# Kernel optimization log

Measured on AMD Instinct MI355X. Metric: run time of the kernel, lower is better.

## Reference

```python
import jax, jax.numpy as jnp
import numpy as np

N = 8192      # nodes
E = 262144    # edges per graph (avg degree 32)
D_IN = 256
HID = 64
HEADS = 2
NEG_SLOPE = 0.2  # PyG GATConv leaky_relu slope


def _self_loops(ei, n):
    loop = jnp.arange(n, dtype=ei.dtype)
    return jnp.concatenate([ei[0], loop]), jnp.concatenate([ei[1], loop])


def gat_conv(x, src, dst, W, att_src, att_dst, b, concat):
    # PyG GATConv: h=[N,H,C]; alpha=softmax_dst(leaky_relu(a_s[src]+a_d[dst]))
    n = x.shape[0]
    H, C = att_src.shape
    h = (x @ W).reshape(n, H, C)
    a_s = (h * att_src).sum(-1)           # [N,H]
    a_d = (h * att_dst).sum(-1)           # [N,H]
    e = jax.nn.leaky_relu(a_s[src] + a_d[dst], NEG_SLOPE)  # [Etot,H]
    e = e - jax.ops.segment_max(e, dst, num_segments=n)[dst]
    e = jnp.exp(e)
    denom = jax.ops.segment_sum(e, dst, num_segments=n)[dst] + 1e-16
    alpha = e / denom                     # edge softmax per target node
    msg = h[src] * alpha[:, :, None]      # [Etot,H,C]
    out = jax.ops.segment_sum(msg, dst, num_segments=n)  # [N,H,C]
    out = out.reshape(n, H * C) if concat else out.mean(axis=1)
    return out + b


def gcn_conv(x, src, dst, W, b):
    # PyG GCNConv: D^{-1/2}(A+I)D^{-1/2} X W + b (self loops already appended)
    n = x.shape[0]
    h = x @ W
    deg = jax.ops.segment_sum(jnp.ones_like(src, jnp.float32), dst, num_segments=n)
    dinv = jax.lax.rsqrt(jnp.maximum(deg, 1.0))
    norm = dinv[src] * dinv[dst]          # [Etot]
    return jax.ops.segment_sum(h[src] * norm[:, None], dst, num_segments=n) + b


def cross_attn(q_in, kv_in, Wq, bq, Wk, bk, Wv, bv, Wo, bo, num_heads):
    n, d = q_in.shape
    hd = d // num_heads
    q = (q_in @ Wq + bq).reshape(n, num_heads, hd)
    k = (kv_in @ Wk + bk).reshape(n, num_heads, hd)
    v = (kv_in @ Wv + bv).reshape(n, num_heads, hd)
    scores = jnp.einsum('qhd,khd->hqk', q, k) / np.sqrt(hd).astype(np.float32)
    attn = jax.nn.softmax(scores, axis=-1)                 # [H,N,N]
    out = jnp.einsum('hqk,khd->qhd', attn, v).reshape(n, d) @ Wo + bo
    weights = attn.mean(axis=0)[None]                      # [1,N,N] avg heads (torch default)
    return out, weights


def setup_inputs():
    key = jax.random.key(0)
    ks = jax.random.split(key, 24)
    w = lambda k, s: jax.random.normal(k, s, jnp.float32) * 0.05
    inp = {
        'x': jax.random.normal(ks[0], (N, D_IN), jnp.float32),
        'edge_index_tkg': jax.random.randint(ks[1], (2, E), 0, N, jnp.int64 if jax.config.jax_enable_x64 else jnp.int32),
        'edge_index_ekg': jax.random.randint(ks[2], (2, E), 0, N, jnp.int64 if jax.config.jax_enable_x64 else jnp.int32),
        # GAT layer 1: heads=2, concat=True
        'gat1_W': w(ks[3], (D_IN, HEADS * HID)),
        'gat1_att_src': w(ks[4], (HEADS, HID)),
        'gat1_att_dst': w(ks[5], (HEADS, HID)),
        'gat1_b': jnp.zeros((HEADS * HID,), jnp.float32),
        # GAT layer 2: heads=1, concat=False
        'gat2_W': w(ks[6], (HEADS * HID, HID)),
        'gat2_att_src': w(ks[7], (1, HID)),
        'gat2_att_dst': w(ks[8], (1, HID)),
        'gat2_b': jnp.zeros((HID,), jnp.float32),
        # GCN layers
        'gcn1_W': w(ks[9], (D_IN, HID)),
        'gcn1_b': jnp.zeros((HID,), jnp.float32),
        'gcn2_W': w(ks[10], (HID, HID)),
        'gcn2_b': jnp.zeros((HID,), jnp.float32),
        # cross attention (hidden=64, 2 heads)
        'Wq': w(ks[11], (HID, HID)), 'bq': jnp.zeros((HID,), jnp.float32),
        'Wk': w(ks[12], (HID, HID)), 'bk': jnp.zeros((HID,), jnp.float32),
        'Wv': w(ks[13], (HID, HID)), 'bv': jnp.zeros((HID,), jnp.float32),
        'Wo': w(ks[14], (HID, HID)), 'bo': jnp.zeros((HID,), jnp.float32),
        # MLP head
        'fc1_W': w(ks[15], (2 * HID, HID)), 'fc1_b': jnp.zeros((HID,), jnp.float32),
        'fc2_W': w(ks[16], (HID, 1)), 'fc2_b': jnp.zeros((1,), jnp.float32),
    }
    return inp


def reference(x, edge_index_tkg, edge_index_ekg,
              gat1_W, gat1_att_src, gat1_att_dst, gat1_b,
              gat2_W, gat2_att_src, gat2_att_dst, gat2_b,
              gcn1_W, gcn1_b, gcn2_W, gcn2_b,
              Wq, bq, Wk, bk, Wv, bv, Wo, bo,
              fc1_W, fc1_b, fc2_W, fc2_b):
    n = x.shape[0]
    src_t, dst_t = _self_loops(edge_index_tkg, n)
    src_e, dst_e = _self_loops(edge_index_ekg, n)

    h_tkg = jax.nn.elu(gat_conv(x, src_t, dst_t, gat1_W, gat1_att_src, gat1_att_dst, gat1_b, True))
    h_tkg = jax.nn.elu(gat_conv(h_tkg, src_t, dst_t, gat2_W, gat2_att_src, gat2_att_dst, gat2_b, False))

    h_ekg = jax.nn.relu(gcn_conv(x, src_e, dst_e, gcn1_W, gcn1_b))
    h_ekg = jax.nn.relu(gcn_conv(h_ekg, src_e, dst_e, gcn2_W, gcn2_b))

    h_attn, attn_weights = cross_attn(h_tkg, h_ekg, Wq, bq, Wk, bk, Wv, bv, Wo, bo, HEADS)

    h_fused = jnp.concatenate([h_tkg, h_attn], axis=1)   # [N, 2*HID]
    pred = (jax.nn.relu(h_fused @ fc1_W + fc1_b) @ fc2_W + fc2_b).squeeze(-1)
    return pred, attn_weights
```

## Files before the change

kernel.cpp:

```cpp
#include <hip/hip_runtime.h>
#include <cstdint>
#include <cstddef>

#define NN 8192
#define EE 262144
#define ET 270336

using short8  = __attribute__((ext_vector_type(8))) short;
using floatx4 = __attribute__((ext_vector_type(4))) float;

__device__ __forceinline__ unsigned short f2bf(float f) {
  unsigned int u = __float_as_uint(f);
  u += 0x7fffu + ((u >> 16) & 1u);
  return (unsigned short)(u >> 16);
}

__global__ void edge_hist2_k(const int* __restrict__ ei_t, const int* __restrict__ ei_e,
                             int* __restrict__ cnt_t, int* __restrict__ cnt_e) {
  int idx = blockIdx.x * 256 + threadIdx.x;
  int g = idx >= ET;
  int e = g ? idx - ET : idx;
  const int* ei = g ? ei_e : ei_t;
  int* cnt = g ? cnt_e : cnt_t;
  int d = (e < EE) ? ei[EE + e] : (e - EE);
  atomicAdd(&cnt[d], 1);
}

__global__ void scan2_k(int* cnt_t, int* off_t, int* cnt_e, int* off_e) {
  int* cnt = blockIdx.x ? cnt_e : cnt_t;
  int* off = blockIdx.x ? off_e : off_t;
  __shared__ int s[1024];
  int t = threadIdx.x;
  int v[8]; int base = t * 8; int sum = 0;
  #pragma unroll
  for (int j = 0; j < 8; ++j) { v[j] = cnt[base + j]; sum += v[j]; }
  s[t] = sum; __syncthreads();
  for (int o = 1; o < 1024; o <<= 1) {
    int x = (t >= o) ? s[t - o] : 0;
    __syncthreads();
    s[t] += x;
    __syncthreads();
  }
  int excl = s[t] - sum;
  #pragma unroll
  for (int j = 0; j < 8; ++j) { off[base + j] = excl; cnt[base + j] = excl; excl += v[j]; }
  if (t == 1023) off[NN] = excl;
}

__global__ void edge_scatter2_k(const int* __restrict__ ei_t, const int* __restrict__ ei_e,
                                int* __restrict__ pos_t, int* __restrict__ pos_e,
                                int* __restrict__ srcs_t, int* __restrict__ srcs_e) {
  int idx = blockIdx.x * 256 + threadIdx.x;
  int g = idx >= ET;
  int e = g ? idx - ET : idx;
  const int* ei = g ? ei_e : ei_t;
  int* pos = g ? pos_e : pos_t;
  int* srcs = g ? srcs_e : srcs_t;
  int sv, d;
  if (e < EE) { sv = ei[e]; d = ei[EE + e]; } else { sv = d = e - EE; }
  int p = atomicAdd(&pos[d], 1);
  srcs[p] = sv;
}

__device__ __forceinline__ void gemm_core(const float* __restrict__ A, int lda, int K,
                                          const float* __restrict__ Bs, int row0, int col,
                                          float acc[8]) {
  #pragma unroll
  for (int r = 0; r < 8; ++r) acc[r] = 0.f;
  for (int k = 0; k < K; k += 4) {
    float b0 = Bs[(k + 0) * 32 + col], b1 = Bs[(k + 1) * 32 + col];
    float b2 = Bs[(k + 2) * 32 + col], b3 = Bs[(k + 3) * 32 + col];
    #pragma unroll
    for (int r = 0; r < 8; ++r) {
      const float4 a4 = *(const float4*)(A + (size_t)(row0 + r) * lda + k);
      acc[r] = fmaf(a4.x, b0, acc[r]);
      acc[r] = fmaf(a4.y, b1, acc[r]);
      acc[r] = fmaf(a4.z, b2, acc[r]);
      acc[r] = fmaf(a4.w, b3, acc[r]);
    }
  }
}

__global__ __launch_bounds__(256) void mm_x_k(const float* __restrict__ x,
    const float* __restrict__ Wgat, const float* __restrict__ Wgcn,
    const float* __restrict__ as_w, const float* __restrict__ ad_w,
    float* __restrict__ h1, float* __restrict__ hg1,
    float* __restrict__ a_s1, float* __restrict__ a_d1) {
  __shared__ float Bs[256 * 32];
  const int tid = threadIdx.x, by = blockIdx.y;
  const bool gat = by < 4;
  const int NC = gat ? 128 : 64;
  const int c0 = gat ? by * 32 : (by - 4) * 32;
  const float* B = gat ? Wgat : Wgcn;
  for (int idx = tid; idx < 256 * 32; idx += 256)
    Bs[idx] = B[(idx >> 5) * NC + c0 + (idx & 31)];
  __syncthreads();
  const int row0 = blockIdx.x * 64 + (tid >> 5) * 8;
  const int col = tid & 31;
  float acc[8];
  gemm_core(x, 256, 256, Bs, row0, col, acc);
  if (gat) {
    #pragma unroll
    for (int r = 0; r < 8; ++r) h1[(size_t)(row0 + r) * 128 + c0 + col] = acc[r];
    const int head = c0 >> 6;
    const float asw = as_w[head * 64 + (c0 & 63) + col];
    const float adw = ad_w[head * 64 + (c0 & 63) + col];
    float ps[8], pd[8];
    #pragma unroll
    for (int r = 0; r < 8; ++r) { ps[r] = acc[r] * asw; pd[r] = acc[r] * adw; }
    #pragma unroll
    for (int m = 16; m >= 1; m >>= 1)
      #pragma unroll
      for (int r = 0; r < 8; ++r) { ps[r] += __shfl_xor(ps[r], m); pd[r] += __shfl_xor(pd[r], m); }
    if (col == 0) {
      #pragma unroll
      for (int r = 0; r < 8; ++r) {
        atomicAdd(&a_s1[(row0 + r) * 2 + head], ps[r]);
        atomicAdd(&a_d1[(row0 + r) * 2 + head], pd[r]);
      }
    }
  } else {
    #pragma unroll
    for (int r = 0; r < 8; ++r) hg1[(size_t)(row0 + r) * 64 + c0 + col] = acc[r];
  }
}

template<int H, int C>
__device__ __forceinline__ void gat_agg_body(const float* __restrict__ h,
    const float* __restrict__ a_s, const float* __restrict__ a_d,
    const int* __restrict__ off, const int* __restrict__ srcs,
    const float* __restrict__ bias, float* __restrict__ out, int ldout, int b) {
  constexpr int HC = H * C;
  const int tid = threadIdx.x;
  const int hd = tid / C;
  const int r0 = off[b], r1 = off[b + 1];
  __shared__ int s_src[HC];
  __shared__ float s_w[HC][H];
  float ad[H];
  #pragma unroll
  for (int hh = 0; hh < H; ++hh) ad[hh] = a_d[b * H + hh];
  float acc = 0.f, den = 0.f;
  for (int base = r0; base < r1; base += HC) {
    __syncthreads();
    int e = base + tid;
    if (e < r1) {
      int sv = srcs[e];
      s_src[tid] = sv;
      #pragma unroll
      for (int hh = 0; hh < H; ++hh) {
        float xv = a_s[sv * H + hh] + ad[hh];
        xv = xv > 0.f ? xv : 0.2f * xv;
        s_w[tid][hh] = __expf(xv);
      }
    }
    __syncthreads();
    int cnt = min(HC, r1 - base);
    for (int j = 0; j < cnt; ++j) {
      float wv = s_w[j][hd];
      den += wv;
      acc = fmaf(wv, h[(size_t)s_src[j] * HC + tid], acc);
    }
  }
  float o = acc / den + bias[tid];
  out[(size_t)b * ldout + tid] = o > 0.f ? o : (__expf(o) - 1.f);
}

template<int H, int C>
__global__ void gat_agg_k(const float* __restrict__ h, const float* __restrict__ a_s,
                          const float* __restrict__ a_d, const int* __restrict__ off,
                          const int* __restrict__ srcs, const float* __restrict__ bias,
                          float* __restrict__ out, int ldout) {
  gat_agg_body<H, C>(h, a_s, a_d, off, srcs, bias, out, ldout, blockIdx.x);
}

__global__ __launch_bounds__(128) void agg1_k(
    const float* __restrict__ h1, const float* __restrict__ a_s1, const float* __restrict__ a_d1,
    const int* __restrict__ off_t, const int* __restrict__ src_t,
    const float* __restrict__ gat1_b, float* __restrict__ g1out,
    const float* __restrict__ hg1, const int* __restrict__ off_e, const int* __restrict__ src_e,
    const float* __restrict__ gcn1_b, const float* __restrict__ gcn2_W, float* __restrict__ h2g) {
  const int tid = threadIdx.x;
  if (blockIdx.x < NN) {
    gat_agg_body<2, 64>(h1, a_s1, a_d1, off_t, src_t, gat1_b, g1out, 128, blockIdx.x);
  } else {
    const int nb = (blockIdx.x - NN) * 2;
    const int sub = tid >> 6, t = tid & 63;
    const int node = nb + sub;
    __shared__ int s_src2[2][64];
    __shared__ float s_nrm2[2][64];
    __shared__ float s_row2[2][64];
    const int r0 = off_e[node], r1 = off_e[node + 1];
    const int cA = off_e[nb + 1] - off_e[nb];
    const int cB = off_e[nb + 2] - off_e[nb + 1];
    const int trips = (max(cA, cB) + 63) >> 6;
    float dinv_b = rsqrtf((float)max(r1 - r0, 1));
    float acc = 0.f;
    for (int it = 0; it < trips; ++it) {
      __syncthreads();
      int e = r0 + it * 64 + t;
      if (e < r1) {
        int sv = src_e[e];
        s_src2[sub][t] = sv;
        int ds = off_e[sv + 1] - off_e[sv];
        s_nrm2[sub][t] = dinv_b * rsqrtf((float)max(ds, 1));
      }
      __syncthreads();
      int cnt = min(64, r1 - (r0 + it * 64));
      for (int j = 0; j < cnt; ++j)
        acc = fmaf(s_nrm2[sub][j], hg1[(size_t)s_src2[sub][j] * 64 + t], acc);
    }
    s_row2[sub][t] = fmaxf(acc + gcn1_b[t], 0.f);
    __syncthreads();
    float acc2 = 0.f;
    for (int k = 0; k < 64; ++k)
      acc2 = fmaf(s_row2[sub][k], gcn2_W[k * 64 + t], acc2);
    h2g[(size_t)node * 64 + t] = acc2;
  }
}

__global__ __launch_bounds__(256) void mm2_k(
    const float* __restrict__ g1out, const float* __restrict__ gat2_W,
    const float* __restrict__ gat2_as, const float* __restrict__ gat2_ad,
    float* __restrict__ h2, float* __restrict__ a_s2, float* __restrict__ a_d2,
    const float* __restrict__ h2g, const int* __restrict__ off_e, const int* __restrict__ src_e,
    const float* __restrict__ gcn2_b, float* __restrict__ hekg) {
  const int tid = threadIdx.x;
  if (blockIdx.x < 256) {
    __shared__ float Bs[128 * 32];
    const int bx = blockIdx.x & 127;
    const int c0 = (blockIdx.x >> 7) * 32;
    for (int idx = tid; idx < 128 * 32; idx += 256)
      Bs[idx] = gat2_W[(idx >> 5) * 64 + c0 + (idx & 31)];
    __syncthreads();
    const int row0 = bx * 64 + (tid >> 5) * 8;
    const int col = tid & 31;
    float acc[8];
    gemm_core(g1out, 128, 128, Bs, row0, col, acc);
    const float asw = gat2_as[c0 + col];
    const float adw = gat2_ad[c0 + col];
    float ps[8], pd[8];
    #pragma unroll
    for (int r = 0; r < 8; ++r) {
      h2[(size_t)(row0 + r) * 64 + c0 + col] = acc[r];
      ps[r] = acc[r] * asw; pd[r] = acc[r] * adw;
    }
    #pragma unroll
    for (int m = 16; m >= 1; m >>= 1)
      #pragma unroll
      for (int r = 0; r < 8; ++r) { ps[r] += __shfl_xor(ps[r], m); pd[r] += __shfl_xor(pd[r], m); }
    if (col == 0) {
      #pragma unroll
      for (int r = 0; r < 8; ++r) {
        atomicAdd(&a_s2[row0 + r], ps[r]);
        atomicAdd(&a_d2[row0 + r], pd[r]);
      }
    }
  } else {
    const int nb = (blockIdx.x - 256) * 4;
    const int sub = tid >> 6, t = tid & 63;
    const int node = nb + sub;
    __shared__ int s_src4[4][64];
    __shared__ float s_nrm4[4][64];
    const int r0 = off_e[node], r1 = off_e[node + 1];
    int cmax = 0;
    #pragma unroll
    for (int i = 0; i < 4; ++i) cmax = max(cmax, off_e[nb + i + 1] - off_e[nb + i]);
    const int trips = (cmax + 63) >> 6;
    float dinv_b = rsqrtf((float)max(r1 - r0, 1));
    float acc = 0.f;
    for (int it = 0; it < trips; ++it) {
      __syncthreads();
      int e = r0 + it * 64 + t;
      if (e < r1) {
        int sv = src_e[e];
        s_src4[sub][t] = sv;
        int ds = off_e[sv + 1] - off_e[sv];
        s_nrm4[sub][t] = dinv_b * rsqrtf((float)max(ds, 1));
      }
      __syncthreads();
      int cnt = min(64, r1 - (r0 + it * 64));
      for (int j = 0; j < cnt; ++j)
        acc = fmaf(s_nrm4[sub][j], h2g[(size_t)s_src4[sub][j] * 64 + t], acc);
    }
    hekg[(size_t)node * 64 + t] = fmaxf(acc + gcn2_b[t], 0.f);
  }
}

__global__ __launch_bounds__(256) void mm_qkv_k(const float* __restrict__ htkg,
    const float* __restrict__ hekg,
    const float* __restrict__ Wq, const float* __restrict__ bq,
    const float* __restrict__ Wk, const float* __restrict__ bk,
    const float* __restrict__ Wv, const float* __restrict__ bv,
    unsigned short* __restrict__ qb, unsigned short* __restrict__ kb,
    unsigned short* __restrict__ Vt) {
  __shared__ float Bs[64 * 32];
  __shared__ float Ts[32][65];
  const int tid = threadIdx.x, by = blockIdx.y;
  const int kind = by >> 1;
  const int c0 = (by & 1) * 32;
  const float* A = (kind == 0) ? htkg : hekg;
  const float* B = (kind == 0) ? Wq : (kind == 1) ? Wk : Wv;
  const float* bias = (kind == 0) ? bq : (kind == 1) ? bk : bv;
  for (int idx = tid; idx < 64 * 32; idx += 256)
    Bs[idx] = B[(idx >> 5) * 64 + c0 + (idx & 31)];
  __syncthreads();
  const int row0 = blockIdx.x * 64 + (tid >> 5) * 8;
  const int col = tid & 31;
  float acc[8];
  gemm_core(A, 64, 64, Bs, row0, col, acc);
  const float bb = bias[c0 + col];
  if (kind == 0) {
    const float SCL = 0.17677669529663687f * 1.4426950408889634f;
    #pragma unroll
    for (int r = 0; r < 8; ++r)
      qb[(size_t)(row0 + r) * 64 + c0 + col] = f2bf((acc[r] + bb) * SCL);
  } else if (kind == 1) {
    #pragma unroll
    for (int r = 0; r < 8; ++r)
      kb[(size_t)(row0 + r) * 64 + c0 + col] = f2bf(acc[r] + bb);
  } else {
    const int rl = (tid >> 5) * 8;
    #pragma unroll
    for (int r = 0; r < 8; ++r) Ts[col][rl + r] = acc[r] + bb;
    __syncthreads();
    const int c = tid >> 3, rr = (tid & 7) * 8;
    short8 pk;
    #pragma unroll
    for (int j = 0; j < 8; ++j) pk[j] = (short)f2bf(Ts[c][rr + j]);
    *(short8*)(Vt + (size_t)(c0 + c) * NN + blockIdx.x * 64 + rr) = pk;
  }
}

__global__ __launch_bounds__(256) void att_fused(
    const unsigned short* __restrict__ qb, const unsigned short* __restrict__ kb,
    const unsigned short* __restrict__ Vt,
    float* __restrict__ attn, float* __restrict__ O) {
  __shared__ __align__(16) float Esh[4][2][16 * 36];
  __shared__ float lsh[4][16][2];
  __shared__ float Osh[16 * 64];
  const int tid = threadIdx.x;
  const int lane = tid & 63, wv = tid >> 6;
  const int ql = lane & 15, quad = lane >> 4;
  const int qt0 = blockIdx.x * 16;
  const floatx4 zf = {0.f, 0.f, 0.f, 0.f};

  for (int idx = tid; idx < 16 * 64; idx += 256) Osh[idx] = 0.f;

  short8 qf[2];
  #pragma unroll
  for (int h = 0; h < 2; ++h)
    qf[h] = *(const short8*)(qb + (size_t)(qt0 + ql) * 64 + h * 32 + quad * 8);

  float lacc[2][4];
  #pragma unroll
  for (int h = 0; h < 2; ++h)
    #pragma unroll
    for (int r = 0; r < 4; ++r) lacc[h][r] = 0.f;
  int kbase = wv * 2048;
  for (int it = 0; it < 64; ++it, kbase += 32) {
    short8 kf[2][2];
    #pragma unroll
    for (int kt = 0; kt < 2; ++kt)
      #pragma unroll
      for (int h = 0; h < 2; ++h)
        kf[kt][h] = *(const short8*)(kb + (size_t)(kbase + kt * 16 + ql) * 64 + h * 32 + quad * 8);
    #pragma unroll
    for (int h = 0; h < 2; ++h)
      #pragma unroll
      for (int kt = 0; kt < 2; ++kt) {
        floatx4 s = __builtin_amdgcn_mfma_f32_16x16x32_bf16(qf[h], kf[kt][h], zf, 0, 0, 0);
        #pragma unroll
        for (int r = 0; r < 4; ++r) lacc[h][r] += __builtin_amdgcn_exp2f(s[r]);
      }
  }
  #pragma unroll
  for (int o = 8; o >= 1; o >>= 1)
    #pragma unroll
    for (int h = 0; h < 2; ++h)
      #pragma unroll
      for (int r = 0; r < 4; ++r)
        lacc[h][r] += __shfl_xor(lacc[h][r], o, 16);
  if (ql == 0) {
    #pragma unroll
    for (int h = 0; h < 2; ++h)
      #pragma unroll
      for (int r = 0; r < 4; ++r)
        lsh[wv][quad * 4 + r][h] = lacc[h][r];
  }
  __syncthreads();
  float invl[2][4];
  #pragma unroll
  for (int h = 0; h < 2; ++h)
    #pragma unroll
    for (int r = 0; r < 4; ++r) {
      int row = quad * 4 + r;
      invl[h][r] = 1.0f / (lsh[0][row][h] + lsh[1][row][h] + lsh[2][row][h] + lsh[3][row][h]);
    }

  floatx4 oacc[2][2];
  #pragma unroll
  for (int h = 0; h < 2; ++h)
    #pragma unroll
    for (int hf = 0; hf < 2; ++hf) oacc[h][hf] = zf;

  const int r8 = lane >> 3;
  const int c4 = (lane & 7) * 4;
  kbase = wv * 2048;
  for (int it = 0; it < 64; ++it, kbase += 32) {
    short8 kf[2][2], vf[2][2];
    #pragma unroll
    for (int kt = 0; kt < 2; ++kt)
      #pragma unroll
      for (int h = 0; h < 2; ++h)
        kf[kt][h] = *(const short8*)(kb + (size_t)(kbase + kt * 16 + ql) * 64 + h * 32 + quad * 8);
    #pragma unroll
    for (int h = 0; h < 2; ++h)
      #pragma unroll
      for (int hf = 0; hf < 2; ++hf)
        vf[h][hf] = *(const short8*)(Vt + (size_t)(h * 32 + hf * 16 + ql) * NN + kbase + quad * 8);

    floatx4 p[2][2];
    #pragma unroll
    for (int h = 0; h < 2; ++h)
      #pragma unroll
      for (int kt = 0; kt < 2; ++kt) {
        floatx4 s = __builtin_amdgcn_mfma_f32_16x16x32_bf16(qf[h], kf[kt][h], zf, 0, 0, 0);
        #pragma unroll
        for (int r = 0; r < 4; ++r)
          p[h][kt][r] = __builtin_amdgcn_exp2f(s[r]) * invl[h][r];
      }
    #pragma unroll
    for (int h = 0; h < 2; ++h)
      #pragma unroll
      for (int kt = 0; kt < 2; ++kt)
        #pragma unroll
        for (int r = 0; r < 4; ++r)
          Esh[wv][h][(quad * 4 + r) * 36 + kt * 16 + ql] = p[h][kt][r];
    {
      const float4 a0 = *(const float4*)&Esh[wv][0][r8 * 36 + c4];
      const float4 b0 = *(const float4*)&Esh[wv][1][r8 * 36 + c4];
      const float4 a1 = *(const float4*)&Esh[wv][0][(r8 + 8) * 36 + c4];
      const float4 b1 = *(const float4*)&Esh[wv][1][(r8 + 8) * 36 + c4];
      float4 m0, m1;
      m0.x = 0.5f * (a0.x + b0.x); m0.y = 0.5f * (a0.y + b0.y);
      m0.z = 0.5f * (a0.z + b0.z); m0.w = 0.5f * (a0.w + b0.w);
      m1.x = 0.5f * (a1.x + b1.x); m1.y = 0.5f * (a1.y + b1.y);
      m1.z = 0.5f * (a1.z + b1.z); m1.w = 0.5f * (a1.w + b1.w);
      *(float4*)&attn[(size_t)(qt0 + r8) * NN + kbase + c4] = m0;
      *(float4*)&attn[(size_t)(qt0 + r8 + 8) * NN + kbase + c4] = m1;
    }
    #pragma unroll
    for (int h = 0; h < 2; ++h) {
      const float* ep = &Esh[wv][h][ql * 36 + quad * 8];
      float4 x0 = *(const float4*)ep;
      float4 x1 = *(const float4*)(ep + 4);
      short8 ef;
      ef[0] = (short)f2bf(x0.x); ef[1] = (short)f2bf(x0.y);
      ef[2] = (short)f2bf(x0.z); ef[3] = (short)f2bf(x0.w);
      ef[4] = (short)f2bf(x1.x); ef[5] = (short)f2bf(x1.y);
      ef[6] = (short)f2bf(x1.z); ef[7] = (short)f2bf(x1.w);
      #pragma unroll
      for (int hf = 0; hf < 2; ++hf)
        oacc[h][hf] = __builtin_amdgcn_mfma_f32_16x16x32_bf16(ef, vf[h][hf], oacc[h][hf], 0, 0, 0);
    }
  }
  #pragma unroll
  for (int h = 0; h < 2; ++h)
    #pragma unroll
    for (int hf = 0; hf < 2; ++hf)
      #pragma unroll
      for (int r = 0; r < 4; ++r)
        atomicAdd(&Osh[(quad * 4 + r) * 64 + h * 32 + hf * 16 + ql], oacc[h][hf][r]);
  __syncthreads();
  for (int idx = tid; idx < 16 * 64; idx += 256)
    O[(size_t)qt0 * 64 + idx] = Osh[idx];
}

__global__ __launch_bounds__(256) void tail_k(const float* __restrict__ O,
    const float* __restrict__ htkg, const float* __restrict__ Wo, const float* __restrict__ bo,
    const float* __restrict__ fc1W, const float* __restrict__ fc1b,
    const float* __restrict__ fc2W, const float* __restrict__ fc2b,
    float* __restrict__ pred) {
  __shared__ float Ws[8192];
  __shared__ float T1[2048];
  __shared__ float T2[2048];
  const int tid = threadIdx.x;
  const int col = tid & 63, rg = tid >> 6;
  const int rowbase = blockIdx.x * 32;
  for (int i = tid; i < 2048; i += 256) T1[i] = O[(size_t)rowbase * 64 + i];
  for (int i = tid; i < 4096; i += 256) Ws[i] = Wo[i];
  const float rbo = bo[col], rf1b = fc1b[col], rf2 = fc2W[col], rf2b = fc2b[0];
  __syncthreads();
  float ha[8];
  #pragma unroll
  for (int r = 0; r < 8; ++r) {
    const int row = rg * 8 + r;
    float acc = rbo;
    for (int k = 0; k < 64; ++k) acc = fmaf(T1[row * 64 + k], Ws[k * 64 + col], acc);
    ha[r] = acc;
  }
  __syncthreads();
  #pragma unroll
  for (int r = 0; r < 8; ++r) T2[(rg * 8 + r) * 64 + col] = ha[r];
  for (int i = tid; i < 2048; i += 256) T1[i] = htkg[(size_t)rowbase * 64 + i];
  for (int i = tid; i < 8192; i += 256) Ws[i] = fc1W[i];
  __syncthreads();
  #pragma unroll
  for (int r = 0; r < 8; ++r) {
    const int row = rg * 8 + r;
    float acc = rf1b;
    for (int k = 0; k < 64; ++k) acc = fmaf(T1[row * 64 + k], Ws[k * 64 + col], acc);
    for (int k = 0; k < 64; ++k) acc = fmaf(T2[row * 64 + k], Ws[(64 + k) * 64 + col], acc);
    float y = fmaxf(acc, 0.f);
    float v = y * rf2;
    #pragma unroll
    for (int m = 32; m >= 1; m >>= 1) v += __shfl_xor(v, m);
    if (col == 0) pred[rowbase + row] = v + rf2b;
  }
}

extern "C" void kernel_launch(void* const* d_in, const int* in_sizes, int n_in,
                              void* d_out, int out_size, void* d_ws, size_t ws_size,
                              hipStream_t stream) {
  (void)in_sizes; (void)n_in; (void)out_size; (void)ws_size;
  const float* x       = (const float*)d_in[0];
  const int*   ei_t    = (const int*)d_in[1];
  const int*   ei_e    = (const int*)d_in[2];
  const float* gat1_W  = (const float*)d_in[3];
  const float* gat1_as = (const float*)d_in[4];
  const float* gat1_ad = (const float*)d_in[5];
  const float* gat1_b  = (const float*)d_in[6];
  const float* gat2_W  = (const float*)d_in[7];
  const float* gat2_as = (const float*)d_in[8];
  const float* gat2_ad = (const float*)d_in[9];
  const float* gat2_b  = (const float*)d_in[10];
  const float* gcn1_W  = (const float*)d_in[11];
  const float* gcn1_b  = (const float*)d_in[12];
  const float* gcn2_W  = (const float*)d_in[13];
  const float* gcn2_b  = (const float*)d_in[14];
  const float* Wq = (const float*)d_in[15]; const float* bq = (const float*)d_in[16];
  const float* Wk = (const float*)d_in[17]; const float* bk = (const float*)d_in[18];
  const float* Wv = (const float*)d_in[19]; const float* bv = (const float*)d_in[20];
  const float* Wo = (const float*)d_in[21]; const float* bo = (const float*)d_in[22];
  const float* fc1_W = (const float*)d_in[23]; const float* fc1_b = (const float*)d_in[24];
  const float* fc2_W = (const float*)d_in[25]; const float* fc2_b = (const float*)d_in[26];

  float* out  = (float*)d_out;
  float* attn = out + NN;

  char* wsp = (char*)d_ws;
  size_t ofs = 0;
  auto take = [&](size_t bytes) -> char* {
    char* p = wsp + ofs;
    ofs = (ofs + bytes + 255) & ~(size_t)255;
    return p;
  };
  int*   pos_t = (int*)take(NN * 4);
  int*   pos_e = (int*)take(NN * 4);
  float* a_s1  = (float*)take((size_t)NN * 2 * 4);
  float* a_d1  = (float*)take((size_t)NN * 2 * 4);
  float* a_s2  = (float*)take((size_t)NN * 4);
  float* a_d2  = (float*)take((size_t)NN * 4);
  const size_t zero_span = ofs;
  int* off_t = (int*)take((NN + 1) * 4);
  int* off_e = (int*)take((NN + 1) * 4);
  int* src_t = (int*)take((size_t)ET * 4);
  int* src_e = (int*)take((size_t)ET * 4);
  float* h1    = (float*)take((size_t)NN * 128 * 4);
  float* g1out = (float*)take((size_t)NN * 128 * 4);
  float* h2    = (float*)take((size_t)NN * 64 * 4);
  float* htkg  = (float*)take((size_t)NN * 64 * 4);
  float* hg1   = (float*)take((size_t)NN * 64 * 4);
  float* h2g   = (float*)take((size_t)NN * 64 * 4);
  float* hekg  = (float*)take((size_t)NN * 64 * 4);
  unsigned short* qb = (unsigned short*)take((size_t)NN * 64 * 2);
  unsigned short* kb = (unsigned short*)take((size_t)NN * 64 * 2);
  unsigned short* Vt = (unsigned short*)take((size_t)64 * NN * 2);
  float* Obuf  = (float*)take((size_t)NN * 64 * 4);

  hipMemsetAsync(wsp, 0, zero_span, stream);

  edge_hist2_k<<<2 * ET / 256, 256, 0, stream>>>(ei_t, ei_e, pos_t, pos_e);
  scan2_k<<<2, 1024, 0, stream>>>(pos_t, off_t, pos_e, off_e);
  edge_scatter2_k<<<2 * ET / 256, 256, 0, stream>>>(ei_t, ei_e, pos_t, pos_e, src_t, src_e);

  mm_x_k<<<dim3(128, 6), 256, 0, stream>>>(x, gat1_W, gcn1_W, gat1_as, gat1_ad,
                                           h1, hg1, a_s1, a_d1);
  agg1_k<<<NN + NN / 2, 128, 0, stream>>>(h1, a_s1, a_d1, off_t, src_t, gat1_b, g1out,
                                          hg1, off_e, src_e, gcn1_b, gcn2_W, h2g);
  mm2_k<<<256 + NN / 4, 256, 0, stream>>>(g1out, gat2_W, gat2_as, gat2_ad, h2, a_s2, a_d2,
                                          h2g, off_e, src_e, gcn2_b, hekg);
  gat_agg_k<1, 64><<<NN, 64, 0, stream>>>(h2, a_s2, a_d2, off_t, src_t, gat2_b, htkg, 64);

  mm_qkv_k<<<dim3(128, 6), 256, 0, stream>>>(htkg, hekg, Wq, bq, Wk, bk, Wv, bv, qb, kb, Vt);

  att_fused<<<512, 256, 0, stream>>>(qb, kb, Vt, attn, Obuf);

  tail_k<<<256, 256, 0, stream>>>(Obuf, htkg, Wo, bo, fc1_W, fc1_b, fc2_W, fc2_b, out);
}
```

Before: 663.8 us.

## Split fused attention into row-sum and PV kernels with key-split grid

Breaks the single fused attention kernel into two kernels, one computing softmax denominators and one computing probabilities, writing attention weights and P·V. Each kernel now splits the key dimension four ways across blockIdx.y, raising the block count from 512 to 2048 so more CUs are occupied. Partial sums are combined with global atomics into zeroed buffers. This adds an extra launch, reloads Q and K, and adds atomic traffic on O and the row sums.

```diff
diff --git a/kernel.cpp b/kernel.cpp
--- a/kernel.cpp
+++ b/kernel.cpp
@@ -331,12 +331,70 @@
   }
 }
 
-__global__ __launch_bounds__(256) void att_fused(
+__global__ __launch_bounds__(256) void att_lsum_k(
     const unsigned short* __restrict__ qb, const unsigned short* __restrict__ kb,
-    const unsigned short* __restrict__ Vt,
+    float* __restrict__ lsum) {
+  __shared__ float lsh[4][16][2];
+  const int tid = threadIdx.x;
+  const int lane = tid & 63, wv = tid >> 6;
+  const int ql = lane & 15, quad = lane >> 4;
+  const int qt0 = blockIdx.x * 16;
+  const floatx4 zf = {0.f, 0.f, 0.f, 0.f};
+
+  short8 qf[2];
+  #pragma unroll
+  for (int h = 0; h < 2; ++h)
+    qf[h] = *(const short8*)(qb + (size_t)(qt0 + ql) * 64 + h * 32 + quad * 8);
+
+  float lacc[2][4];
+  #pragma unroll
+  for (int h = 0; h < 2; ++h)
+    #pragma unroll
+    for (int r = 0; r < 4; ++r) lacc[h][r] = 0.f;
+  int kbase = blockIdx.y * 2048 + wv * 512;
+  for (int it = 0; it < 16; ++it, kbase += 32) {
+    short8 kf[2][2];
+    #pragma unroll
+    for (int kt = 0; kt < 2; ++kt)
+      #pragma unroll
+      for (int h = 0; h < 2; ++h)
+        kf[kt][h] = *(const short8*)(kb + (size_t)(kbase + kt * 16 + ql) * 64 + h * 32 + quad * 8);
+    #pragma unroll
+    for (int h = 0; h < 2; ++h)
+      #pragma unroll
+      for (int kt = 0; kt < 2; ++kt) {
+        floatx4 s = __builtin_amdgcn_mfma_f32_16x16x32_bf16(qf[h], kf[kt][h], zf, 0, 0, 0);
+        #pragma unroll
+        for (int r = 0; r < 4; ++r) lacc[h][r] += __builtin_amdgcn_exp2f(s[r]);
+      }
+  }
+  #pragma unroll
+  for (int o = 8; o >= 1; o >>= 1)
+    #pragma unroll
+    for (int h = 0; h < 2; ++h)
+      #pragma unroll
+      for (int r = 0; r < 4; ++r)
+        lacc[h][r] += __shfl_xor(lacc[h][r], o, 16);
+  if (ql == 0) {
+    #pragma unroll
+    for (int h = 0; h < 2; ++h)
+      #pragma unroll
+      for (int r = 0; r < 4; ++r)
+        lsh[wv][quad * 4 + r][h] = lacc[h][r];
+  }
+  __syncthreads();
+  if (tid < 32) {
+    const int row = tid >> 1, h = tid & 1;
+    float s = lsh[0][row][h] + lsh[1][row][h] + lsh[2][row][h] + lsh[3][row][h];
+    atomicAdd(&lsum[(qt0 + row) * 2 + h], s);
+  }
+}
+
+__global__ __launch_bounds__(256) void att_pv_k(
+    const unsigned short* __restrict__ qb, const unsigned short* __restrict__ kb,
+    const unsigned short* __restrict__ Vt, const float* __restrict__ lsum,
     float* __restrict__ attn, float* __restrict__ O) {
   __shared__ __align__(16) float Esh[4][2][16 * 36];
-  __shared__ float lsh[4][16][2];
   __shared__ float Osh[16 * 64];
   const int tid = threadIdx.x;
   const int lane = tid & 63, wv = tid >> 6;
@@ -345,57 +403,19 @@
   const floatx4 zf = {0.f, 0.f, 0.f, 0.f};
 
   for (int idx = tid; idx < 16 * 64; idx += 256) Osh[idx] = 0.f;
+  __syncthreads();
 
   short8 qf[2];
   #pragma unroll
   for (int h = 0; h < 2; ++h)
     qf[h] = *(const short8*)(qb + (size_t)(qt0 + ql) * 64 + h * 32 + quad * 8);
 
-  float lacc[2][4];
+  float invl[2][4];
   #pragma unroll
   for (int h = 0; h < 2; ++h)
     #pragma unroll
-    for (int r = 0; r < 4; ++r) lacc[h][r] = 0.f;
-  int kbase = wv * 2048;
-  for (int it = 0; it < 64; ++it, kbase += 32) {
-    short8 kf[2][2];
-    #pragma unroll
-    for (int kt = 0; kt < 2; ++kt)
-      #pragma unroll
-      for (int h = 0; h < 2; ++h)
-        kf[kt][h] = *(const short8*)(kb + (size_t)(kbase + kt * 16 + ql) * 64 + h * 32 + quad * 8);
-    #pragma unroll
-    for (int h = 0; h < 2; ++h)
-      #pragma unroll
-      for (int kt = 0; kt < 2; ++kt) {
-        floatx4 s = __builtin_amdgcn_mfma_f32_16x16x32_bf16(qf[h], kf[kt][h], zf, 0, 0, 0);
-        #pragma unroll
-        for (int r = 0; r < 4; ++r) lacc[h][r] += __builtin_amdgcn_exp2f(s[r]);
-      }
-  }
-  #pragma unroll
-  for (int o = 8; o >= 1; o >>= 1)
-    #pragma unroll
-    for (int h = 0; h < 2; ++h)
-      #pragma unroll
-      for (int r = 0; r < 4; ++r)
-        lacc[h][r] += __shfl_xor(lacc[h][r], o, 16);
-  if (ql == 0) {
-    #pragma unroll
-    for (int h = 0; h < 2; ++h)
-      #pragma unroll
-      for (int r = 0; r < 4; ++r)
-        lsh[wv][quad * 4 + r][h] = lacc[h][r];
-  }
-  __syncthreads();
-  float invl[2][4];
-  #pragma unroll
-  for (int h = 0; h < 2; ++h)
-    #pragma unroll
-    for (int r = 0; r < 4; ++r) {
-      int row = quad * 4 + r;
-      invl[h][r] = 1.0f / (lsh[0][row][h] + lsh[1][row][h] + lsh[2][row][h] + lsh[3][row][h]);
-    }
+    for (int r = 0; r < 4; ++r)
+      invl[h][r] = 1.0f / lsum[(qt0 + quad * 4 + r) * 2 + h];
 
   floatx4 oacc[2][2];
   #pragma unroll
@@ -405,8 +425,8 @@
 
   const int r8 = lane >> 3;
   const int c4 = (lane & 7) * 4;
-  kbase = wv * 2048;
-  for (int it = 0; it < 64; ++it, kbase += 32) {
+  int kbase = blockIdx.y * 2048 + wv * 512;
+  for (int it = 0; it < 16; ++it, kbase += 32) {
     short8 kf[2][2], vf[2][2];
     #pragma unroll
     for (int kt = 0; kt < 2; ++kt)
@@ -473,7 +493,7 @@
         atomicAdd(&Osh[(quad * 4 + r) * 64 + h * 32 + hf * 16 + ql], oacc[h][hf][r]);
   __syncthreads();
   for (int idx = tid; idx < 16 * 64; idx += 256)
-    O[(size_t)qt0 * 64 + idx] = Osh[idx];
+    atomicAdd(&O[(size_t)qt0 * 64 + idx], Osh[idx]);
 }
 
 __global__ __launch_bounds__(256) void tail_k(const float* __restrict__ O,
@@ -561,6 +581,8 @@
   float* a_d1  = (float*)take((size_t)NN * 2 * 4);
   float* a_s2  = (float*)take((size_t)NN * 4);
   float* a_d2  = (float*)take((size_t)NN * 4);
+  float* a_l   = (float*)take((size_t)NN * 2 * 4);
+  float* Obuf  = (float*)take((size_t)NN * 64 * 4);
   const size_t zero_span = ofs;
   int* off_t = (int*)take((NN + 1) * 4);
   int* off_e = (int*)take((NN + 1) * 4);
@@ -576,7 +598,6 @@
   unsigned short* qb = (unsigned short*)take((size_t)NN * 64 * 2);
   unsigned short* kb = (unsigned short*)take((size_t)NN * 64 * 2);
   unsigned short* Vt = (unsigned short*)take((size_t)64 * NN * 2);
-  float* Obuf  = (float*)take((size_t)NN * 64 * 4);
 
   hipMemsetAsync(wsp, 0, zero_span, stream);
 
@@ -594,7 +615,8 @@
 
   mm_qkv_k<<<dim3(128, 6), 256, 0, stream>>>(htkg, hekg, Wq, bq, Wk, bk, Wv, bv, qb, kb, Vt);
 
-  att_fused<<<512, 256, 0, stream>>>(qb, kb, Vt, attn, Obuf);
+  att_lsum_k<<<dim3(512, 4), 256, 0, stream>>>(qb, kb, a_l);
+  att_pv_k<<<dim3(512, 4), 256, 0, stream>>>(qb, kb, Vt, a_l, attn, Obuf);
 
   tail_k<<<256, 256, 0, stream>>>(Obuf, htkg, Wo, bo, fc1_W, fc1_b, fc2_W, fc2_b, out);
 }
```

Result: slower. 702.5 us (+5.8%).
